# Optimization experiments

Hardware: AMD Instinct MI355X
Metric: run time of the kernel (lower is better)

Reference implementation:

```python
import jax, jax.numpy as jnp
import numpy as np

TIMESTEPS = 100  # init kwarg: timesteps
CLIP_MAX = 1e10


def setup_inputs() -> dict:
    key = jax.random.key(0)
    kR, kT, krho, kb = jax.random.split(key, 4)
    N, M, C = 1024, 64, 4
    R = jax.random.uniform(kR, (N, M, M), dtype=jnp.float32)
    R = R / jnp.sum(R, axis=2, keepdims=True)   # row-stochastic mobility matrices
    T = jax.random.uniform(kT, (N, C, C), dtype=jnp.float32)
    T = T / jnp.sum(T, axis=2, keepdims=True)   # row-stochastic compartment transitions
    rho0 = jax.random.uniform(krho, (N, M, C), dtype=jnp.float32) * 0.01
    beta = jax.random.uniform(kb, (N,), dtype=jnp.float32) * 0.2
    return {"R": R, "T": T, "rho0": rho0, "beta": beta}


def _infect_prob(neff, ntot, beta):
    # py0-style contact infection: infectious compartment index 1
    ninf = neff[..., 1]                                    # (N, M, M)
    x = beta[:, None, None] * ninf / ntot[:, None, :]      # (N, M, M)
    return 1.0 - jnp.exp(jnp.sum(jnp.log(1.0 - x), axis=2))  # (N, M)


def reference(R, T, rho0, beta):
    N, M, C = rho0.shape
    # ntot is loop-invariant (same math as recomputing per step)
    ntot = jnp.sum(R, axis=1)                              # (N, M)
    # faithful to tf.reshape(tf.transpose(R), (-1, M, M, 1)): full-reverse transpose then reshape
    Rt = jnp.transpose(R).reshape(N, M, M, 1)
    e0 = jnp.zeros((C,), rho0.dtype).at[0].set(1.0)        # one-hot: new infections -> compartment 0

    def step(rho, _):
        neff = rho.reshape(N, M, 1, C) * Rt                # (N, M, M, C)
        p = _infect_prob(neff, ntot, beta)                 # (N, M)
        new_inf = (1.0 - jnp.sum(rho, axis=-1)) * jnp.einsum('ijk,ik->ij', R, p)
        rho_new = jnp.einsum('ijk,ikl->ijl', rho, T) + new_inf[:, :, None] * e0
        rho_new = jnp.clip(rho_new, 0.0, CLIP_MAX)
        return rho_new, rho                                # trajectory records pre-update state

    _, trajs = jax.lax.scan(step, rho0, None, length=TIMESTEPS)
    return trajs                                           # (timesteps, N, M, C)
```

## Files before the change

kernel.cpp:

```cpp
#include <hip/hip_runtime.h>

typedef __attribute__((ext_vector_type(2))) float f32x2;

#define NS 1024
#define MM 64
#define CC 4
#define NSTEPS 100
#define CLIPMAX 1e10f

__device__ __forceinline__ float rdlane(float v, int k) {
    return __uint_as_float(__builtin_amdgcn_readlane(__float_as_uint(v), k));
}
__device__ __forceinline__ float sfirst(float v) {
    return __uint_as_float(__builtin_amdgcn_readfirstlane(__float_as_uint(v)));
}

extern "C" __global__
__attribute__((amdgpu_flat_work_group_size(64, 64), amdgpu_waves_per_eu(1, 1)))
void metapop_kernel(
    const float* __restrict__ R,
    const float* __restrict__ T,
    const float* __restrict__ rho0,
    const float* __restrict__ beta,
    float* __restrict__ out)
{
    const int n    = blockIdx.x;
    const int lane = threadIdx.x;

    __shared__ float pbuf[MM];

    const float* Rn = R + (size_t)n * (MM * MM);

    f32x2 Rrow2[32];
    {
        const float4* p4 = (const float4*)(Rn + lane * MM);
        #pragma unroll
        for (int q = 0; q < 16; ++q) {
            float4 v = p4[q];
            Rrow2[2*q]   = (f32x2){v.x, v.y};
            Rrow2[2*q+1] = (f32x2){v.z, v.w};
        }
    }

    float nt = 0.f;
    #pragma unroll
    for (int i = 0; i < MM; ++i) nt += Rn[i * MM + lane];
    const float binv = beta[n] / nt;

    float S1 = 0.f, S2 = 0.f, S3 = 0.f, S4 = 0.f;
    {
        const int q     = n >> 4;
        const int a     = ((n & 15) << 2) + (lane >> 4);
        const int sbase = (lane & 15) << 6;
        #pragma unroll
        for (int j = 0; j < MM; ++j) {
            float g  = R[(size_t)(sbase + j) * (MM * MM) + a * MM + q]
                     * rdlane(binv, j);
            float g2 = g * g;
            S1 += g;  S2 += g2;  S3 += g2 * g;  S4 += g2 * g2;
        }
    }
    const float T1 = S1, T2 = 0.5f * S2,
                T3 = (1.f / 3.f) * S3, T4 = 0.25f * S4;

    #pragma unroll
    for (int q = 0; q < 32; ++q) asm volatile("" : "+v"(Rrow2[q]));

    float tt[CC][CC];
    {
        const float* Tn = T + n * (CC * CC);
        #pragma unroll
        for (int k = 0; k < CC; ++k)
            #pragma unroll
            for (int l = 0; l < CC; ++l)
                tt[k][l] = sfirst(Tn[k * CC + l]);
    }

    float rh[CC];
    {
        float4 v = *(const float4*)(rho0 + (size_t)n * (MM * CC) + lane * CC);
        rh[0] = v.x; rh[1] = v.y; rh[2] = v.z; rh[3] = v.w;
    }

    float* ob = out + (size_t)n * (MM * CC) + lane * CC;
    const size_t stride = (size_t)NS * MM * CC;

    for (int step = 0; step < NSTEPS; ++step) {
        *(float4*)(ob + (size_t)step * stride) =
            make_float4(rh[0], rh[1], rh[2], rh[3]);

        const float r1 = rh[1];
        const float h  = T1 + r1 * (T2 + r1 * (T3 + r1 * T4));
        const float p  = 1.f - __expf(-(r1 * h));

        pbuf[lane] = p;

        f32x2 a0 = {0.f, 0.f}, a1 = {0.f, 0.f}, a2 = {0.f, 0.f}, a3 = {0.f, 0.f};
        {
            const float4* pb4 = (const float4*)pbuf;
            #pragma unroll
            for (int q = 0; q < 4; ++q) {
                float4 pv;
                pv = pb4[q];
                a0 += Rrow2[2*q]      * (f32x2){pv.x, pv.y};
                a0 += Rrow2[2*q + 1]  * (f32x2){pv.z, pv.w};
                pv = pb4[q + 4];
                a1 += Rrow2[2*q + 8]  * (f32x2){pv.x, pv.y};
                a1 += Rrow2[2*q + 9]  * (f32x2){pv.z, pv.w};
                pv = pb4[q + 8];
                a2 += Rrow2[2*q + 16] * (f32x2){pv.x, pv.y};
                a2 += Rrow2[2*q + 17] * (f32x2){pv.z, pv.w};
                pv = pb4[q + 12];
                a3 += Rrow2[2*q + 24] * (f32x2){pv.x, pv.y};
                a3 += Rrow2[2*q + 25] * (f32x2){pv.z, pv.w};
            }
        }
        const f32x2 aa = (a0 + a1) + (a2 + a3);
        const float ssum = aa.x + aa.y;
        const float sr   = (rh[0] + rh[1]) + (rh[2] + rh[3]);
        const float ninf = (1.f - sr) * ssum;

        float nr[CC];
        #pragma unroll
        for (int l = 0; l < CC; ++l) {
            float v = rh[0] * tt[0][l] + rh[1] * tt[1][l]
                    + rh[2] * tt[2][l] + rh[3] * tt[3][l];
            if (l == 0) v += ninf;
            nr[l] = fminf(fmaxf(v, 0.f), CLIPMAX);
        }
        #pragma unroll
        for (int l = 0; l < CC; ++l) rh[l] = nr[l];
    }
}

extern "C" void kernel_launch(void* const* d_in, const int* in_sizes, int n_in,
                              void* d_out, int out_size, void* d_ws, size_t ws_size,
                              hipStream_t stream) {
    const float* R    = (const float*)d_in[0];
    const float* T    = (const float*)d_in[1];
    const float* rho0 = (const float*)d_in[2];
    const float* beta = (const float*)d_in[3];
    float* out = (float*)d_out;
    hipLaunchKernelGGL(metapop_kernel, dim3(NS), dim3(64), 0, stream,
                       R, T, rho0, beta, out);
}
```

Baseline: 54.95 us.

## Software-pipeline infection probability with double-buffered LDS and register prefetch

Computes the next step's compartment-1 state and infection probability before the current step's matvec, writes it to a double-buffered shared array, and prefetches all 64 probabilities into registers for the next iteration. This takes the LDS write-then-read round trip off the serial per-step dependency chain, because rh1 does not depend on new infections. In exchange it holds 64 more VGPRs, and it relies on the single 64-lane wave for LDS visibility since there is no barrier.

```diff
diff --git a/kernel.cpp b/kernel.cpp
--- a/kernel.cpp
+++ b/kernel.cpp
@@ -27,7 +27,7 @@
     const int n    = blockIdx.x;
     const int lane = threadIdx.x;
 
-    __shared__ float pbuf[MM];
+    __shared__ float pbuf[2][MM];
 
     const float* Rn = R + (size_t)n * (MM * MM);
 
@@ -76,60 +76,76 @@
                 tt[k][l] = sfirst(Tn[k * CC + l]);
     }
 
-    float rh[CC];
+    float rh0, rh1, rh2, rh3;
     {
         float4 v = *(const float4*)(rho0 + (size_t)n * (MM * CC) + lane * CC);
-        rh[0] = v.x; rh[1] = v.y; rh[2] = v.z; rh[3] = v.w;
+        rh0 = v.x; rh1 = v.y; rh2 = v.z; rh3 = v.w;
     }
 
     float* ob = out + (size_t)n * (MM * CC) + lane * CC;
     const size_t stride = (size_t)NS * MM * CC;
 
+    float4 pv[16];
+    {
+        const float h0 = T1 + rh1 * (T2 + rh1 * (T3 + rh1 * T4));
+        pbuf[0][lane] = 1.f - __expf(-(rh1 * h0));
+        const float4* pb4 = (const float4*)pbuf[0];
+        #pragma unroll
+        for (int q = 0; q < 16; ++q) pv[q] = pb4[q];
+    }
+
     for (int step = 0; step < NSTEPS; ++step) {
         *(float4*)(ob + (size_t)step * stride) =
-            make_float4(rh[0], rh[1], rh[2], rh[3]);
+            make_float4(rh0, rh1, rh2, rh3);
 
-        const float r1 = rh[1];
-        const float h  = T1 + r1 * (T2 + r1 * (T3 + r1 * T4));
-        const float p  = 1.f - __expf(-(r1 * h));
+        const float c0 = rh0*tt[0][0] + rh1*tt[1][0] + rh2*tt[2][0] + rh3*tt[3][0];
+        const float c1 = rh0*tt[0][1] + rh1*tt[1][1] + rh2*tt[2][1] + rh3*tt[3][1];
+        const float c2 = rh0*tt[0][2] + rh1*tt[1][2] + rh2*tt[2][2] + rh3*tt[3][2];
+        const float c3 = rh0*tt[0][3] + rh1*tt[1][3] + rh2*tt[2][3] + rh3*tt[3][3];
 
-        pbuf[lane] = p;
+        const float nrh1 = fminf(fmaxf(c1, 0.f), CLIPMAX);
+        const float nrh2 = fminf(fmaxf(c2, 0.f), CLIPMAX);
+        const float nrh3 = fminf(fmaxf(c3, 0.f), CLIPMAX);
+
+        {
+            const float hn = T1 + nrh1 * (T2 + nrh1 * (T3 + nrh1 * T4));
+            pbuf[(step + 1) & 1][lane] = 1.f - __expf(-(nrh1 * hn));
+        }
 
         f32x2 a0 = {0.f, 0.f}, a1 = {0.f, 0.f}, a2 = {0.f, 0.f}, a3 = {0.f, 0.f};
-        {
-            const float4* pb4 = (const float4*)pbuf;
-            #pragma unroll
-            for (int q = 0; q < 4; ++q) {
-                float4 pv;
-                pv = pb4[q];
-                a0 += Rrow2[2*q]      * (f32x2){pv.x, pv.y};
-                a0 += Rrow2[2*q + 1]  * (f32x2){pv.z, pv.w};
-                pv = pb4[q + 4];
-                a1 += Rrow2[2*q + 8]  * (f32x2){pv.x, pv.y};
-                a1 += Rrow2[2*q + 9]  * (f32x2){pv.z, pv.w};
-                pv = pb4[q + 8];
-                a2 += Rrow2[2*q + 16] * (f32x2){pv.x, pv.y};
-                a2 += Rrow2[2*q + 17] * (f32x2){pv.z, pv.w};
-                pv = pb4[q + 12];
-                a3 += Rrow2[2*q + 24] * (f32x2){pv.x, pv.y};
-                a3 += Rrow2[2*q + 25] * (f32x2){pv.z, pv.w};
-            }
+        #pragma unroll
+        for (int q = 0; q < 4; ++q) {
+            float4 pvv;
+            pvv = pv[q];
+            a0 += Rrow2[2*q]      * (f32x2){pvv.x, pvv.y};
+            a0 += Rrow2[2*q + 1]  * (f32x2){pvv.z, pvv.w};
+            pvv = pv[q + 4];
+            a1 += Rrow2[2*q + 8]  * (f32x2){pvv.x, pvv.y};
+            a1 += Rrow2[2*q + 9]  * (f32x2){pvv.z, pvv.w};
+            pvv = pv[q + 8];
+            a2 += Rrow2[2*q + 16] * (f32x2){pvv.x, pvv.y};
+            a2 += Rrow2[2*q + 17] * (f32x2){pvv.z, pvv.w};
+            pvv = pv[q + 12];
+            a3 += Rrow2[2*q + 24] * (f32x2){pvv.x, pvv.y};
+            a3 += Rrow2[2*q + 25] * (f32x2){pvv.z, pvv.w};
         }
         const f32x2 aa = (a0 + a1) + (a2 + a3);
         const float ssum = aa.x + aa.y;
-        const float sr   = (rh[0] + rh[1]) + (rh[2] + rh[3]);
+        const float sr   = (rh0 + rh1) + (rh2 + rh3);
         const float ninf = (1.f - sr) * ssum;
+        const float nrh0 = fminf(fmaxf(c0 + ninf, 0.f), CLIPMAX);
 
-        float nr[CC];
-        #pragma unroll
-        for (int l = 0; l < CC; ++l) {
-            float v = rh[0] * tt[0][l] + rh[1] * tt[1][l]
-                    + rh[2] * tt[2][l] + rh[3] * tt[3][l];
-            if (l == 0) v += ninf;
-            nr[l] = fminf(fmaxf(v, 0.f), CLIPMAX);
+        {
+            const float4* pb4 = (const float4*)pbuf[(step + 1) & 1];
+            #pragma unroll
+            for (int q = 0; q < 16; ++q) pv[q] = pb4[q];
+            #pragma unroll
+            for (int q = 0; q < 16; ++q)
+                asm volatile("" : "+v"(pv[q].x), "+v"(pv[q].y),
+                                  "+v"(pv[q].z), "+v"(pv[q].w));
         }
-        #pragma unroll
-        for (int l = 0; l < CC; ++l) rh[l] = nr[l];
+
+        rh0 = nrh0; rh1 = nrh1; rh2 = nrh2; rh3 = nrh3;
     }
 }
 
```

Result: slower. 64.01 us (+16.5%).

## Duplicate each population across two blocks that split trajectory stores by step parity

Applied to the files above, without the earlier changes.

Launches two blocks per population. Each block recomputes the full 100-step recurrence redundantly, but only writes the output for steps of its parity, which halves the store traffic per block. Waves-per-EU is raised to 2 so the duplicated blocks can share a SIMD and overlap compute with stores. The cost is twice the compute and twice the R loads, plus tighter register limits that could spill the 64-float R row.

```diff
diff --git a/kernel.cpp b/kernel.cpp
--- a/kernel.cpp
+++ b/kernel.cpp
@@ -16,7 +16,7 @@
 }
 
 extern "C" __global__
-__attribute__((amdgpu_flat_work_group_size(64, 64), amdgpu_waves_per_eu(1, 1)))
+__attribute__((amdgpu_flat_work_group_size(64, 64), amdgpu_waves_per_eu(2, 2)))
 void metapop_kernel(
     const float* __restrict__ R,
     const float* __restrict__ T,
@@ -24,8 +24,10 @@
     const float* __restrict__ beta,
     float* __restrict__ out)
 {
-    const int n    = blockIdx.x;
-    const int lane = threadIdx.x;
+    const int bid    = blockIdx.x;
+    const int n      = bid >> 1;
+    const int parity = bid & 1;
+    const int lane   = threadIdx.x;
 
     __shared__ float pbuf[MM];
 
@@ -76,20 +78,21 @@
                 tt[k][l] = sfirst(Tn[k * CC + l]);
     }
 
-    float rh[CC];
+    float rh0, rh1, rh2, rh3;
     {
         float4 v = *(const float4*)(rho0 + (size_t)n * (MM * CC) + lane * CC);
-        rh[0] = v.x; rh[1] = v.y; rh[2] = v.z; rh[3] = v.w;
+        rh0 = v.x; rh1 = v.y; rh2 = v.z; rh3 = v.w;
     }
 
     float* ob = out + (size_t)n * (MM * CC) + lane * CC;
     const size_t stride = (size_t)NS * MM * CC;
 
     for (int step = 0; step < NSTEPS; ++step) {
-        *(float4*)(ob + (size_t)step * stride) =
-            make_float4(rh[0], rh[1], rh[2], rh[3]);
+        if ((step & 1) == parity)
+            *(float4*)(ob + (size_t)step * stride) =
+                make_float4(rh0, rh1, rh2, rh3);
 
-        const float r1 = rh[1];
+        const float r1 = rh1;
         const float h  = T1 + r1 * (T2 + r1 * (T3 + r1 * T4));
         const float p  = 1.f - __expf(-(r1 * h));
 
@@ -117,19 +120,17 @@
         }
         const f32x2 aa = (a0 + a1) + (a2 + a3);
         const float ssum = aa.x + aa.y;
-        const float sr   = (rh[0] + rh[1]) + (rh[2] + rh[3]);
+        const float sr   = (rh0 + rh1) + (rh2 + rh3);
         const float ninf = (1.f - sr) * ssum;
 
-        float nr[CC];
-        #pragma unroll
-        for (int l = 0; l < CC; ++l) {
-            float v = rh[0] * tt[0][l] + rh[1] * tt[1][l]
-                    + rh[2] * tt[2][l] + rh[3] * tt[3][l];
-            if (l == 0) v += ninf;
-            nr[l] = fminf(fmaxf(v, 0.f), CLIPMAX);
-        }
-        #pragma unroll
-        for (int l = 0; l < CC; ++l) rh[l] = nr[l];
+        const float c0 = rh0*tt[0][0] + rh1*tt[1][0] + rh2*tt[2][0] + rh3*tt[3][0] + ninf;
+        const float c1 = rh0*tt[0][1] + rh1*tt[1][1] + rh2*tt[2][1] + rh3*tt[3][1];
+        const float c2 = rh0*tt[0][2] + rh1*tt[1][2] + rh2*tt[2][2] + rh3*tt[3][2];
+        const float c3 = rh0*tt[0][3] + rh1*tt[1][3] + rh2*tt[2][3] + rh3*tt[3][3];
+        rh0 = fminf(fmaxf(c0, 0.f), CLIPMAX);
+        rh1 = fminf(fmaxf(c1, 0.f), CLIPMAX);
+        rh2 = fminf(fmaxf(c2, 0.f), CLIPMAX);
+        rh3 = fminf(fmaxf(c3, 0.f), CLIPMAX);
     }
 }
 
@@ -141,6 +142,6 @@
     const float* rho0 = (const float*)d_in[2];
     const float* beta = (const float*)d_in[3];
     float* out = (float*)d_out;
-    hipLaunchKernelGGL(metapop_kernel, dim3(NS), dim3(64), 0, stream,
+    hipLaunchKernelGGL(metapop_kernel, dim3(2 * NS), dim3(64), 0, stream,
                        R, T, rho0, beta, out);
 }
```

After: 81.22 us. +47.8%, slower.

## Double-buffer infection probabilities and compute next step's p ahead of matvec

Applied to the files above, without the earlier changes.

Converts the series for p (1-exp(-x)) into a direct polynomial via cumulant-to-moment coefficients, removing the exp per step. The probability for the next step is computed early from the new rho1 and written into an alternate LDS buffer, so the LDS write and the matvec read of the current step are decoupled and the loop is manually unrolled by two with ping-pong buffers. This shortens the serial dependency chain per step but changes the approximation (truncated 4th-order polynomial of 1-exp) which may alter numerics.

```diff
diff --git a/kernel.cpp b/kernel.cpp
--- a/kernel.cpp
+++ b/kernel.cpp
@@ -27,7 +27,8 @@
     const int n    = blockIdx.x;
     const int lane = threadIdx.x;
 
-    __shared__ float pbuf[MM];
+    __shared__ float bufA[MM];
+    __shared__ float bufB[MM];
 
     const float* Rn = R + (size_t)n * (MM * MM);
 
@@ -60,8 +61,13 @@
             S1 += g;  S2 += g2;  S3 += g2 * g;  S4 += g2 * g2;
         }
     }
-    const float T1 = S1, T2 = 0.5f * S2,
-                T3 = (1.f / 3.f) * S3, T4 = 0.25f * S4;
+    const float c1 = S1, c2 = 0.5f * S2, c3 = (1.f / 3.f) * S3, c4 = 0.25f * S4;
+    const float c1sq = c1 * c1;
+    const float d1 = c1;
+    const float d2 = c2 - 0.5f * c1sq;
+    const float d3 = c3 - c1 * c2 + (1.f / 6.f) * c1sq * c1;
+    const float d4 = c4 - c1 * c3 - 0.5f * c2 * c2 + 0.5f * c1sq * c2
+                   - (1.f / 24.f) * c1sq * c1sq;
 
     #pragma unroll
     for (int q = 0; q < 32; ++q) asm volatile("" : "+v"(Rrow2[q]));
@@ -76,28 +82,35 @@
                 tt[k][l] = sfirst(Tn[k * CC + l]);
     }
 
-    float rh[CC];
+    float rh0, rh1, rh2, rh3;
     {
         float4 v = *(const float4*)(rho0 + (size_t)n * (MM * CC) + lane * CC);
-        rh[0] = v.x; rh[1] = v.y; rh[2] = v.z; rh[3] = v.w;
+        rh0 = v.x; rh1 = v.y; rh2 = v.z; rh3 = v.w;
     }
 
     float* ob = out + (size_t)n * (MM * CC) + lane * CC;
     const size_t stride = (size_t)NS * MM * CC;
 
-    for (int step = 0; step < NSTEPS; ++step) {
+    bufA[lane] = rh1 * (d1 + rh1 * (d2 + rh1 * (d3 + rh1 * d4)));
+
+    auto body = [&](const float* __restrict__ RD, float* __restrict__ WR,
+                    int step) {
         *(float4*)(ob + (size_t)step * stride) =
-            make_float4(rh[0], rh[1], rh[2], rh[3]);
+            make_float4(rh0, rh1, rh2, rh3);
 
-        const float r1 = rh[1];
-        const float h  = T1 + r1 * (T2 + r1 * (T3 + r1 * T4));
-        const float p  = 1.f - __expf(-(r1 * h));
+        const float c1s = rh0*tt[0][1] + rh1*tt[1][1] + rh2*tt[2][1] + rh3*tt[3][1];
+        const float nrh1 = fminf(fmaxf(c1s, 0.f), CLIPMAX);
+        WR[lane] = nrh1 * (d1 + nrh1 * (d2 + nrh1 * (d3 + nrh1 * d4)));
 
-        pbuf[lane] = p;
+        const float c2s = rh0*tt[0][2] + rh1*tt[1][2] + rh2*tt[2][2] + rh3*tt[3][2];
+        const float c3s = rh0*tt[0][3] + rh1*tt[1][3] + rh2*tt[2][3] + rh3*tt[3][3];
+        const float c0s = rh0*tt[0][0] + rh1*tt[1][0] + rh2*tt[2][0] + rh3*tt[3][0];
+        const float nrh2 = fminf(fmaxf(c2s, 0.f), CLIPMAX);
+        const float nrh3 = fminf(fmaxf(c3s, 0.f), CLIPMAX);
 
         f32x2 a0 = {0.f, 0.f}, a1 = {0.f, 0.f}, a2 = {0.f, 0.f}, a3 = {0.f, 0.f};
         {
-            const float4* pb4 = (const float4*)pbuf;
+            const float4* pb4 = (const float4*)RD;
             #pragma unroll
             for (int q = 0; q < 4; ++q) {
                 float4 pv;
@@ -117,19 +130,17 @@
         }
         const f32x2 aa = (a0 + a1) + (a2 + a3);
         const float ssum = aa.x + aa.y;
-        const float sr   = (rh[0] + rh[1]) + (rh[2] + rh[3]);
+        const float sr   = (rh0 + rh1) + (rh2 + rh3);
         const float ninf = (1.f - sr) * ssum;
 
-        float nr[CC];
-        #pragma unroll
-        for (int l = 0; l < CC; ++l) {
-            float v = rh[0] * tt[0][l] + rh[1] * tt[1][l]
-                    + rh[2] * tt[2][l] + rh[3] * tt[3][l];
-            if (l == 0) v += ninf;
-            nr[l] = fminf(fmaxf(v, 0.f), CLIPMAX);
-        }
-        #pragma unroll
-        for (int l = 0; l < CC; ++l) rh[l] = nr[l];
+        rh0 = fminf(fmaxf(c0s + ninf, 0.f), CLIPMAX);
+        rh1 = nrh1; rh2 = nrh2; rh3 = nrh3;
+    };
+
+    #pragma unroll 1
+    for (int it = 0; it < NSTEPS / 2; ++it) {
+        body(bufA, bufB, 2 * it);
+        body(bufB, bufA, 2 * it + 1);
     }
 }
 
```

Measured after the change: 64.34 us. 1.17x slower.
